# Kernel optimization log

Measured on AMD Instinct MI355X. Metric: run time of the kernel, lower is better.

Reference implementation:

```python
import jax, jax.numpy as jnp
import numpy as np


def _deform_unfold(feat, offset):
    """Deformable 3x3 unfold with bilinear sampling, zero padding outside.
    feat: [B,C,H,W], offset: [B,2K,H,W] (y,x per point). Returns [B,C,K,H,W]."""
    B, C, H, W = feat.shape
    K = offset.shape[1] // 2
    off = offset.reshape(B, K, 2, H, W)
    # 3x3 kernel grid, dilation 1, padding 1 -> relative taps in {-1,0,1}
    ky = (jnp.arange(K) // 3 - 1).astype(feat.dtype)
    kx = (jnp.arange(K) % 3 - 1).astype(feat.dtype)
    hh = jnp.arange(H, dtype=feat.dtype)
    ww = jnp.arange(W, dtype=feat.dtype)
    py = hh[None, None, :, None] + ky[None, :, None, None] + off[:, :, 0]  # [B,K,H,W]
    px = ww[None, None, None, :] + kx[None, :, None, None] + off[:, :, 1]  # [B,K,H,W]
    y0 = jnp.floor(py)
    x0 = jnp.floor(px)
    fy = py - y0  # frac weights
    fx = px - x0
    y0i = y0.astype(jnp.int32)
    x0i = x0.astype(jnp.int32)

    def gather(yi, xi):
        valid = ((yi >= 0) & (yi < H) & (xi >= 0) & (xi < W)).astype(feat.dtype)
        yc = jnp.clip(yi, 0, H - 1)
        xc = jnp.clip(xi, 0, W - 1)
        v = jax.vmap(lambda f, yy, xx: f[:, yy, xx])(feat, yc, xc)  # [B,C,K,H,W]
        return v * valid[:, None]

    w00 = ((1 - fy) * (1 - fx))[:, None]
    w01 = ((1 - fy) * fx)[:, None]
    w10 = (fy * (1 - fx))[:, None]
    w11 = (fy * fx)[:, None]
    return (gather(y0i, x0i) * w00 + gather(y0i, x0i + 1) * w01 +
            gather(y0i + 1, x0i) * w10 + gather(y0i + 1, x0i + 1) * w11)


def setup_inputs() -> dict:
    key = jax.random.key(0)
    ks = jax.random.split(key, 8)
    B, C, H, W = 4, 256, 64, 64
    Ci, P = 128, 9
    x = jax.random.normal(ks[0], (B, C, H, W), jnp.float32)
    offset = jax.random.normal(ks[1], (B, 2 * P, H, W), jnp.float32)
    std = 0.01  # normal_init(std=0.01)
    Wq = jax.random.normal(ks[2], (Ci, C), jnp.float32) * std
    Wk = jax.random.normal(ks[3], (Ci, C), jnp.float32) * std
    Wv = jax.random.normal(ks[4], (Ci, C), jnp.float32) * std
    Wo = jax.random.normal(ks[5], (Ci,), jnp.float32) * std
    bq = jnp.zeros((Ci,), jnp.float32)
    bk = jnp.zeros((Ci,), jnp.float32)
    bv = jnp.zeros((Ci,), jnp.float32)
    bo = jnp.zeros((1,), jnp.float32)
    return {"x": x, "offset": offset, "Wq": Wq, "bq": bq, "Wk": Wk, "bk": bk,
            "Wv": Wv, "bv": bv, "Wo": Wo, "bo": bo}


def reference(x, offset, Wq, bq, Wk, bk, Wv, bv, Wo, bo):
    # 1x1 conv projections
    q = jnp.einsum('bchw,oc->bohw', x, Wq) + bq[None, :, None, None]
    k = jnp.einsum('bchw,oc->bohw', x, Wk) + bk[None, :, None, None]
    v = jnp.einsum('bchw,oc->bohw', x, Wv) + bv[None, :, None, None]
    qu = _deform_unfold(q, offset)  # [B,Ci,K,H,W]
    ku = _deform_unfold(k, offset)  # [B,Ci,K,H,W]
    vu = _deform_unfold(v, offset)  # [B,Ci,K,H,W]
    # per-pixel KxK attention: query [K,Ci] @ key [Ci,K]
    scores = jnp.einsum('bcihw,bcjhw->bijhw', qu, ku)  # [B,K,K,H,W]
    attn = jax.nn.softmax(scores, axis=2)
    # attn [K,K] @ value [K,Ci]
    out_v = jnp.einsum('bijhw,bcjhw->bcihw', attn, vu)  # [B,Ci,K,H,W]
    # conv_out: 1x1 conv Ci->1 over the value, then sigmoid -> [B,K,H,W]
    out = jnp.einsum('bcihw,c->bihw', out_v, Wo) + bo[0]
    return jax.nn.sigmoid(out)
```

## Files before the change

### kernel.cpp

```cpp
#include <hip/hip_runtime.h>

typedef unsigned short u16;
typedef unsigned int u32;

#define B_   4
#define C_   256
#define CI_  128
#define H_   64
#define W_   64
#define NPB_ 4096
#define NP_  16384
#define K_   9
#define MROWS_ 272

typedef __attribute__((ext_vector_type(8))) __bf16 bf16x8_t;
typedef __attribute__((ext_vector_type(4))) float f32x4_t;
typedef __attribute__((ext_vector_type(2))) float f32x2_t;
typedef __attribute__((ext_vector_type(4))) u32 u32x4;

#define GLD(dst, p, immstr) \
    asm volatile("global_load_dwordx4 %0, %1, off offset:" immstr \
                 : "=v"(dst) : "v"(p))

__device__ __forceinline__ float bf2f_lo(u32 w) {
    union { u32 i; float f; } x; x.i = w << 16; return x.f;
}
__device__ __forceinline__ float bf2f_hi(u32 w) {
    union { u32 i; float f; } x; x.i = w & 0xffff0000u; return x.f;
}
__device__ __forceinline__ u16 f2bf(float f) {
    union { float f; u32 i; } x; x.f = f;
    u32 lsb = (x.i >> 16) & 1u;
    return (u16)((x.i + 0x7fffu + lsb) >> 16);
}
__device__ __forceinline__ void acc8p(f32x2_t* f, u32x4 v, f32x2_t w2) {
    f32x2_t p;
    p.x = bf2f_lo(v[0]); p.y = bf2f_hi(v[0]); f[0] += w2 * p;
    p.x = bf2f_lo(v[1]); p.y = bf2f_hi(v[1]); f[1] += w2 * p;
    p.x = bf2f_lo(v[2]); p.y = bf2f_hi(v[2]); f[2] += w2 * p;
    p.x = bf2f_lo(v[3]); p.y = bf2f_hi(v[3]); f[3] += w2 * p;
}

__global__ void k0b_prep(const float* __restrict__ Wq, const float* __restrict__ bq,
                         const float* __restrict__ Wk, const float* __restrict__ bk,
                         const float* __restrict__ Wv, const float* __restrict__ bv,
                         const float* __restrict__ Wo,
                         u16* __restrict__ Wt, float* __restrict__ bias) {
    const int o = blockIdx.x;
    const int c = threadIdx.x;
    u16 val;
    if (o < 128) {
        val = f2bf(Wq[o * C_ + c]);
        if (c == 0) bias[o] = bq[o];
    } else if (o < 256) {
        val = f2bf(Wk[(o - 128) * C_ + c]);
        if (c == 0) bias[o] = bk[o - 128];
    } else if (o == 256) {
        float s = 0.f;
        #pragma unroll 8
        for (int oo = 0; oo < CI_; ++oo)
            s += Wo[oo] * Wv[oo * C_ + c];
        val = f2bf(s);
        if (c == 0) {
            float ts = 0.f;
            #pragma unroll 8
            for (int oo = 0; oo < CI_; ++oo) ts += Wo[oo] * bv[oo];
            bias[256] = ts;
        }
    } else {
        val = 0;
        if (c == 0) bias[o] = 0.f;
    }
    const int mt = o >> 4, l16 = o & 15;
    const int kk = c >> 5, g = (c >> 3) & 3, e = c & 7;
    Wt[(size_t)((mt * 8 + kk) * 64 + g * 16 + l16) * 8 + e] = val;
}

__global__ __launch_bounds__(512) void k1_proj(
    const float* __restrict__ x, const u16* __restrict__ Wt,
    const float* __restrict__ bias,
    u16* __restrict__ qk, float* __restrict__ vs) {
    __shared__ u16 xs[16][272];
    const int t = threadIdx.x;
    const int l = t & 63;
    const int w = t >> 6;
    const int lane16 = l & 15;
    const int g = l >> 4;
    const int p0 = blockIdx.x * 16;
    const int b = p0 >> 12;
    const int pin = p0 & 4095;

    const int mts[3] = {2 * w, 2 * w + 1, 16};

    u32x4 afr[8][3];
    #pragma unroll
    for (int n = 0; n < 3; ++n) {
        const u16* pA = Wt + ((size_t)(mts[n] * 8) * 64 + l) * 8;
        const u16* pB = pA + 4 * 64 * 8;
        GLD(afr[0][n], pA, "0");    GLD(afr[1][n], pA, "1024");
        GLD(afr[2][n], pA, "2048"); GLD(afr[3][n], pA, "3072");
        GLD(afr[4][n], pB, "0");    GLD(afr[5][n], pB, "1024");
        GLD(afr[6][n], pB, "2048"); GLD(afr[7][n], pB, "3072");
    }

    {
        const int spx = t & 15, cg = t >> 4;
        const float* src = x + (size_t)(b * C_ + cg * 8) * NPB_ + pin + spx;
        float v[8];
        #pragma unroll
        for (int i = 0; i < 8; ++i) v[i] = src[(size_t)i * NPB_];
        uint4 pk;
        pk.x = (u32)f2bf(v[0]) | ((u32)f2bf(v[1]) << 16);
        pk.y = (u32)f2bf(v[2]) | ((u32)f2bf(v[3]) << 16);
        pk.z = (u32)f2bf(v[4]) | ((u32)f2bf(v[5]) << 16);
        pk.w = (u32)f2bf(v[6]) | ((u32)f2bf(v[7]) << 16);
        *reinterpret_cast<uint4*>(&xs[spx][cg * 8]) = pk;
    }
    __syncthreads();
    asm volatile("s_waitcnt vmcnt(0)" ::: "memory");
    __builtin_amdgcn_sched_barrier(0);

    f32x4_t acc[3];
    #pragma unroll
    for (int n = 0; n < 3; ++n)
        #pragma unroll
        for (int r = 0; r < 4; ++r)
            acc[n][r] = bias[mts[n] * 16 + g * 4 + r];

    #pragma unroll
    for (int kk = 0; kk < 8; ++kk) {
        const bf16x8_t bv = *reinterpret_cast<const bf16x8_t*>(&xs[lane16][kk * 32 + g * 8]);
        #pragma unroll
        for (int n = 0; n < 3; ++n) {
            const bf16x8_t av = __builtin_bit_cast(bf16x8_t, afr[kk][n]);
            acc[n] = __builtin_amdgcn_mfma_f32_16x16x32_bf16(av, bv, acc[n], 0, 0, 0);
        }
    }

    const int px = p0 + lane16;
    u16* qrow = qk + (size_t)px * C_;
    #pragma unroll
    for (int n = 0; n < 2; ++n) {
        const int mt = mts[n];
        u32* dst = reinterpret_cast<u32*>(qrow + mt * 16 + g * 4);
        dst[0] = (u32)f2bf(acc[n][0]) | ((u32)f2bf(acc[n][1]) << 16);
        dst[1] = (u32)f2bf(acc[n][2]) | ((u32)f2bf(acc[n][3]) << 16);
    }
    if (w == 0 && g == 0) vs[px] = acc[2][0];
}

__global__ __launch_bounds__(256) void k2_attn(
    const float* __restrict__ off, const u16* __restrict__ qk,
    const float* __restrict__ vs, const float* __restrict__ bo,
    float* __restrict__ out) {
    __shared__ f32x4_t red[3][64];
    const int t = threadIdx.x;
    const int l = t & 63;
    const int w = t >> 6;
    const int bid = blockIdx.x;
    const int pixel = (bid & 7) * (NP_ / 8) + (bid >> 3);
    const int b = pixel >> 12;
    const int rem = pixel & 4095;
    const int y = rem >> 6, xx = rem & 63;
    const int l16 = l & 15;
    const int tap = (l16 < K_) ? l16 : (K_ - 1);
    const int g = l >> 4;

    const float* offb = off + ((size_t)b * (2 * K_) + 2 * tap) * NPB_ + rem;
    const float oy = offb[0];
    const float ox = offb[NPB_];
    const float py = (float)(y + tap / 3 - 1) + oy;
    const float px = (float)(xx + tap % 3 - 1) + ox;
    const float fy0 = floorf(py), fx0 = floorf(px);
    const float fy = py - fy0, fx = px - fx0;
    const int y0 = (int)fy0, x0 = (int)fx0;

    const u16* qkbase = qk + ((size_t)(b << 12)) * C_ + w * 32 + g * 8;
    const float* vsm = vs + (b << 12);

    float wgt[4];
    int ppc[4];
    const u16* bp[4];
    #pragma unroll
    for (int c = 0; c < 4; ++c) {
        const int dy = c >> 1, dx = c & 1;
        const int yi = y0 + dy, xi = x0 + dx;
        const float wv = (dy ? fy : 1.f - fy) * (dx ? fx : 1.f - fx);
        const int ok = (yi >= 0) & (yi < H_) & (xi >= 0) & (xi < W_);
        const int yc = min(max(yi, 0), H_ - 1);
        const int xc = min(max(xi, 0), W_ - 1);
        ppc[c] = yc * W_ + xc;
        wgt[c] = ok ? wv : 0.f;
        bp[c] = qkbase + (size_t)ppc[c] * C_;
    }

    u32x4 gq[4], gk[4];
    #pragma unroll
    for (int c = 0; c < 4; ++c) {
        GLD(gq[c], bp[c], "0");
        GLD(gk[c], bp[c], "256");
    }
    float vsc[4];
    if (w == 0) {
        #pragma unroll
        for (int c = 0; c < 4; ++c) vsc[c] = vsm[ppc[c]];
    }
    asm volatile("s_waitcnt vmcnt(0)" ::: "memory");
    __builtin_amdgcn_sched_barrier(0);

    f32x2_t fq[4], fk[4];
    #pragma unroll
    for (int e = 0; e < 4; ++e) { fq[e] = (f32x2_t){0.f, 0.f}; fk[e] = (f32x2_t){0.f, 0.f}; }
    #pragma unroll
    for (int c = 0; c < 4; ++c) {
        const f32x2_t w2 = {wgt[c], wgt[c]};
        acc8p(fq, gq[c], w2);
        acc8p(fk, gk[c], w2);
    }

    bf16x8_t av, bv;
    #pragma unroll
    for (int e = 0; e < 4; ++e) {
        av[2 * e]     = (__bf16)fk[e].x;
        av[2 * e + 1] = (__bf16)fk[e].y;
        bv[2 * e]     = (__bf16)fq[e].x;
        bv[2 * e + 1] = (__bf16)fq[e].y;
    }
    f32x4_t acc = {0.f, 0.f, 0.f, 0.f};
    acc = __builtin_amdgcn_mfma_f32_16x16x32_bf16(av, bv, acc, 0, 0, 0);

    if (w > 0) red[w - 1][l] = acc;
    __syncthreads();
    if (w != 0) return;

    acc += red[0][l];
    acc += red[1][l];
    acc += red[2][l];

    const float vsu_t = wgt[0] * vsc[0] + wgt[1] * vsc[1] +
                        wgt[2] * vsc[2] + wgt[3] * vsc[3];

    float mx = -1e30f;
    #pragma unroll
    for (int r = 0; r < 4; ++r) {
        const int j = g * 4 + r;
        if (j < K_) mx = fmaxf(mx, acc[r]);
    }
    mx = fmaxf(mx, __shfl_xor(mx, 16, 64));
    mx = fmaxf(mx, __shfl_xor(mx, 32, 64));

    float vj[4];
    #pragma unroll
    for (int r = 0; r < 4; ++r) vj[r] = __shfl(vsu_t, g * 4 + r, 64);

    float den = 0.f, num = 0.f;
    #pragma unroll
    for (int r = 0; r < 4; ++r) {
        const int j = g * 4 + r;
        if (j < K_) {
            const float e = __expf(acc[r] - mx);
            den += e;
            num += e * vj[r];
        }
    }
    den += __shfl_xor(den, 16, 64); den += __shfl_xor(den, 32, 64);
    num += __shfl_xor(num, 16, 64); num += __shfl_xor(num, 32, 64);

    if (l < K_) {
        const float z = num / den + bo[0];
        out[(size_t)b * K_ * NPB_ + (size_t)l * NPB_ + rem] = 1.f / (1.f + __expf(-z));
    }
}

extern "C" void kernel_launch(void* const* d_in, const int* in_sizes, int n_in,
                              void* d_out, int out_size, void* d_ws, size_t ws_size,
                              hipStream_t stream) {
    const float* x   = (const float*)d_in[0];
    const float* off = (const float*)d_in[1];
    const float* Wq  = (const float*)d_in[2];
    const float* bq  = (const float*)d_in[3];
    const float* Wk  = (const float*)d_in[4];
    const float* bk  = (const float*)d_in[5];
    const float* Wv  = (const float*)d_in[6];
    const float* bv  = (const float*)d_in[7];
    const float* Wo  = (const float*)d_in[8];
    const float* bo  = (const float*)d_in[9];
    float* out = (float*)d_out;

    char* ws = (char*)d_ws;
    u16*   qkbuf = (u16*)(ws + 4096);
    float* vsmap = (float*)(ws + 4096 + 8388608);
    u16*   Wt    = (u16*)(ws + 4096 + 8388608 + 65536);
    float* bias  = (float*)(ws + 4096 + 8388608 + 65536 + 139264);

    k0b_prep<<<MROWS_, 256, 0, stream>>>(Wq, bq, Wk, bk, Wv, bv, Wo, Wt, bias);
    k1_proj<<<NP_ / 16, 512, 0, stream>>>(x, Wt, bias, qkbuf, vsmap);
    k2_attn<<<NP_, 256, 0, stream>>>(off, qkbuf, vsmap, bo, out);
}
```

Before: 77.11 us.

## Tile attention kernel over 4x8 pixel blocks with LDS-staged channel-chunked q/k window

The q/k buffer is re-laid out into four channel chunks of 64 (32 q and 32 k channels each). The attention kernel now runs one block per 4x8 pixel tile instead of one block per pixel. Each block stages a 16x20 window of each chunk into shared memory and precomputes the bilinear geometry per pixel and tap. Samples outside the window fall back to global loads. This replaces many scattered global gathers with reuse from shared memory, at the cost of far fewer blocks (512), four chunk passes with barriers, and more registers per thread.

```diff
diff --git a/kernel.cpp b/kernel.cpp
--- a/kernel.cpp
+++ b/kernel.cpp
@@ -12,6 +12,13 @@
 #define NP_  16384
 #define K_   9
 #define MROWS_ 272
+
+#define TH_  4
+#define TW_  8
+#define WH_  16
+#define WW_  20
+#define WPX_ (WH_ * WW_)
+#define CROW_ 68
 
 typedef __attribute__((ext_vector_type(8))) __bf16 bf16x8_t;
 typedef __attribute__((ext_vector_type(4))) float f32x4_t;
@@ -79,7 +86,7 @@
 __global__ __launch_bounds__(512) void k1_proj(
     const float* __restrict__ x, const u16* __restrict__ Wt,
     const float* __restrict__ bias,
-    u16* __restrict__ qk, float* __restrict__ vs) {
+    u16* __restrict__ qkc, float* __restrict__ vs) {
     __shared__ u16 xs[16][272];
     const int t = threadIdx.x;
     const int l = t & 63;
@@ -138,137 +145,184 @@
     }
 
     const int px = p0 + lane16;
-    u16* qrow = qk + (size_t)px * C_;
     #pragma unroll
     for (int n = 0; n < 2; ++n) {
         const int mt = mts[n];
-        u32* dst = reinterpret_cast<u32*>(qrow + mt * 16 + g * 4);
-        dst[0] = (u32)f2bf(acc[n][0]) | ((u32)f2bf(acc[n][1]) << 16);
-        dst[1] = (u32)f2bf(acc[n][2]) | ((u32)f2bf(acc[n][3]) << 16);
+        const u32 lo_ = (u32)f2bf(acc[n][0]) | ((u32)f2bf(acc[n][1]) << 16);
+        const u32 hi_ = (u32)f2bf(acc[n][2]) | ((u32)f2bf(acc[n][3]) << 16);
+        int chunk, base;
+        if (mt < 8) { chunk = mt >> 1; base = (mt & 1) * 16 + g * 4; }
+        else { const int m8 = mt - 8; chunk = m8 >> 1; base = 32 + (m8 & 1) * 16 + g * 4; }
+        u32* dst = reinterpret_cast<u32*>(qkc + ((size_t)(chunk * NP_ + px)) * 64 + base);
+        dst[0] = lo_; dst[1] = hi_;
     }
     if (w == 0 && g == 0) vs[px] = acc[2][0];
 }
 
 __global__ __launch_bounds__(256) void k2_attn(
-    const float* __restrict__ off, const u16* __restrict__ qk,
+    const float* __restrict__ off, const u16* __restrict__ qkc,
     const float* __restrict__ vs, const float* __restrict__ bo,
     float* __restrict__ out) {
-    __shared__ f32x4_t red[3][64];
+    __shared__ u16 cb[WPX_ * CROW_];
+    __shared__ u32 geo[32][9][8];
+    __shared__ float vsl[WPX_];
+
     const int t = threadIdx.x;
     const int l = t & 63;
     const int w = t >> 6;
     const int bid = blockIdx.x;
-    const int pixel = (bid & 7) * (NP_ / 8) + (bid >> 3);
-    const int b = pixel >> 12;
-    const int rem = pixel & 4095;
-    const int y = rem >> 6, xx = rem & 63;
+    const int tid = (bid & 7) * 64 + (bid >> 3);
+    const int b = tid >> 7;
+    const int rr = tid & 127;
+    const int ty0 = (rr >> 3) * TH_;
+    const int tx0 = (rr & 7) * TW_;
+    const int y0w = min(max(ty0 - 6, 0), H_ - WH_);
+    const int x0w = min(max(tx0 - 6, 0), W_ - WW_);
+
+    for (int i = t; i < WPX_; i += 256) {
+        const int gy = y0w + i / WW_, gx = x0w + i % WW_;
+        vsl[i] = vs[(b << 12) + gy * W_ + gx];
+    }
+    for (int e = t; e < 32 * K_; e += 256) {
+        const int px = e / K_, tap = e - px * K_;
+        const int y = ty0 + (px >> 3), x = tx0 + (px & 7);
+        const int rem = y * W_ + x;
+        const float* offb = off + ((size_t)b * (2 * K_) + 2 * tap) * NPB_ + rem;
+        const float oy = offb[0], ox = offb[NPB_];
+        const float pyf = (float)(y + tap / 3 - 1) + oy;
+        const float pxf = (float)(x + tap % 3 - 1) + ox;
+        const float fy0 = floorf(pyf), fx0 = floorf(pxf);
+        const float fy = pyf - fy0, fx = pxf - fx0;
+        const int y0 = (int)fy0, x0 = (int)fx0;
+        #pragma unroll
+        for (int c = 0; c < 4; ++c) {
+            const int dy = c >> 1, dx = c & 1;
+            const int yi = y0 + dy, xi = x0 + dx;
+            const float wv = (dy ? fy : 1.f - fy) * (dx ? fx : 1.f - fx);
+            const int ok = (yi >= 0) & (yi < H_) & (xi >= 0) & (xi < W_);
+            const int yc = min(max(yi, 0), H_ - 1);
+            const int xc = min(max(xi, 0), W_ - 1);
+            const int wy = yc - y0w, wx = xc - x0w;
+            const int in = ((unsigned)wy < WH_) & ((unsigned)wx < WW_);
+            const u32 idx = in ? (u32)(wy * WW_ + wx) : 0xFFFFu;
+            union { float f; u32 i; } wb; wb.f = ok ? wv : 0.f;
+            geo[px][tap][2 * c]     = (idx << 16) | (u32)(yc * W_ + xc);
+            geo[px][tap][2 * c + 1] = wb.i;
+        }
+    }
+    __syncthreads();
+
     const int l16 = l & 15;
     const int tap = (l16 < K_) ? l16 : (K_ - 1);
     const int g = l >> 4;
 
-    const float* offb = off + ((size_t)b * (2 * K_) + 2 * tap) * NPB_ + rem;
-    const float oy = offb[0];
-    const float ox = offb[NPB_];
-    const float py = (float)(y + tap / 3 - 1) + oy;
-    const float px = (float)(xx + tap % 3 - 1) + ox;
-    const float fy0 = floorf(py), fx0 = floorf(px);
-    const float fy = py - fy0, fx = px - fx0;
-    const int y0 = (int)fy0, x0 = (int)fx0;
-
-    const u16* qkbase = qk + ((size_t)(b << 12)) * C_ + w * 32 + g * 8;
-    const float* vsm = vs + (b << 12);
-
-    float wgt[4];
-    int ppc[4];
-    const u16* bp[4];
-    #pragma unroll
+    f32x4_t acc[8];
+    float vsu[8];
+    #pragma unroll
+    for (int ps = 0; ps < 8; ++ps) {
+        acc[ps] = (f32x4_t){0.f, 0.f, 0.f, 0.f};
+        vsu[ps] = 0.f;
+    }
+
     for (int c = 0; c < 4; ++c) {
-        const int dy = c >> 1, dx = c & 1;
-        const int yi = y0 + dy, xi = x0 + dx;
-        const float wv = (dy ? fy : 1.f - fy) * (dx ? fx : 1.f - fx);
-        const int ok = (yi >= 0) & (yi < H_) & (xi >= 0) & (xi < W_);
-        const int yc = min(max(yi, 0), H_ - 1);
-        const int xc = min(max(xi, 0), W_ - 1);
-        ppc[c] = yc * W_ + xc;
-        wgt[c] = ok ? wv : 0.f;
-        bp[c] = qkbase + (size_t)ppc[c] * C_;
-    }
-
-    u32x4 gq[4], gk[4];
-    #pragma unroll
-    for (int c = 0; c < 4; ++c) {
-        GLD(gq[c], bp[c], "0");
-        GLD(gk[c], bp[c], "256");
-    }
-    float vsc[4];
-    if (w == 0) {
-        #pragma unroll
-        for (int c = 0; c < 4; ++c) vsc[c] = vsm[ppc[c]];
-    }
-    asm volatile("s_waitcnt vmcnt(0)" ::: "memory");
-    __builtin_amdgcn_sched_barrier(0);
-
-    f32x2_t fq[4], fk[4];
-    #pragma unroll
-    for (int e = 0; e < 4; ++e) { fq[e] = (f32x2_t){0.f, 0.f}; fk[e] = (f32x2_t){0.f, 0.f}; }
-    #pragma unroll
-    for (int c = 0; c < 4; ++c) {
-        const f32x2_t w2 = {wgt[c], wgt[c]};
-        acc8p(fq, gq[c], w2);
-        acc8p(fk, gk[c], w2);
-    }
-
-    bf16x8_t av, bv;
-    #pragma unroll
-    for (int e = 0; e < 4; ++e) {
-        av[2 * e]     = (__bf16)fk[e].x;
-        av[2 * e + 1] = (__bf16)fk[e].y;
-        bv[2 * e]     = (__bf16)fq[e].x;
-        bv[2 * e + 1] = (__bf16)fq[e].y;
-    }
-    f32x4_t acc = {0.f, 0.f, 0.f, 0.f};
-    acc = __builtin_amdgcn_mfma_f32_16x16x32_bf16(av, bv, acc, 0, 0, 0);
-
-    if (w > 0) red[w - 1][l] = acc;
-    __syncthreads();
-    if (w != 0) return;
-
-    acc += red[0][l];
-    acc += red[1][l];
-    acc += red[2][l];
-
-    const float vsu_t = wgt[0] * vsc[0] + wgt[1] * vsc[1] +
-                        wgt[2] * vsc[2] + wgt[3] * vsc[3];
-
-    float mx = -1e30f;
-    #pragma unroll
-    for (int r = 0; r < 4; ++r) {
-        const int j = g * 4 + r;
-        if (j < K_) mx = fmaxf(mx, acc[r]);
-    }
-    mx = fmaxf(mx, __shfl_xor(mx, 16, 64));
-    mx = fmaxf(mx, __shfl_xor(mx, 32, 64));
-
-    float vj[4];
-    #pragma unroll
-    for (int r = 0; r < 4; ++r) vj[r] = __shfl(vsu_t, g * 4 + r, 64);
-
-    float den = 0.f, num = 0.f;
-    #pragma unroll
-    for (int r = 0; r < 4; ++r) {
-        const int j = g * 4 + r;
-        if (j < K_) {
-            const float e = __expf(acc[r] - mx);
-            den += e;
-            num += e * vj[r];
-        }
-    }
-    den += __shfl_xor(den, 16, 64); den += __shfl_xor(den, 32, 64);
-    num += __shfl_xor(num, 16, 64); num += __shfl_xor(num, 32, 64);
-
-    if (l < K_) {
-        const float z = num / den + bo[0];
-        out[(size_t)b * K_ * NPB_ + (size_t)l * NPB_ + rem] = 1.f / (1.f + __expf(-z));
+        for (int i = t; i < WPX_ * 2; i += 256) {
+            const int wp = i >> 1, half = i & 1;
+            const int gy = y0w + wp / WW_, gx = x0w + wp % WW_;
+            const u16* src = qkc + ((size_t)(c * NP_ + (b << 12) + gy * W_ + gx)) * 64 + half * 32;
+            const uint4 v0 = *reinterpret_cast<const uint4*>(src);
+            const uint4 v1 = *reinterpret_cast<const uint4*>(src + 8);
+            const uint4 v2 = *reinterpret_cast<const uint4*>(src + 16);
+            const uint4 v3 = *reinterpret_cast<const uint4*>(src + 24);
+            u16* d = &cb[wp * CROW_ + half * 32];
+            *reinterpret_cast<uint4*>(d) = v0;
+            *reinterpret_cast<uint4*>(d + 8) = v1;
+            *reinterpret_cast<uint4*>(d + 16) = v2;
+            *reinterpret_cast<uint4*>(d + 24) = v3;
+        }
+        __syncthreads();
+
+        #pragma unroll
+        for (int ps = 0; ps < 8; ++ps) {
+            const int local = w * 8 + ps;
+            const u32x4 ge0 = *reinterpret_cast<const u32x4*>(&geo[local][tap][0]);
+            const u32x4 ge1 = *reinterpret_cast<const u32x4*>(&geo[local][tap][4]);
+            f32x2_t fq[4], fk[4];
+            #pragma unroll
+            for (int e = 0; e < 4; ++e) { fq[e] = (f32x2_t){0.f, 0.f}; fk[e] = (f32x2_t){0.f, 0.f}; }
+            #pragma unroll
+            for (int cn = 0; cn < 4; ++cn) {
+                const u32 gi_w = (cn < 2) ? ge0[2 * cn] : ge1[2 * (cn - 2)];
+                union { u32 i; float f; } wb;
+                wb.i = (cn < 2) ? ge0[2 * cn + 1] : ge1[2 * (cn - 2) + 1];
+                const float wv = wb.f;
+                const u32 idx = gi_w >> 16;
+                u32x4 qv, kv;
+                if (idx != 0xFFFFu) {
+                    const u16* p = &cb[idx * CROW_ + g * 8];
+                    qv = *reinterpret_cast<const u32x4*>(p);
+                    kv = *reinterpret_cast<const u32x4*>(p + 32);
+                    if (c == 0) vsu[ps] += wv * vsl[idx];
+                } else {
+                    const u32 gp = gi_w & 0xFFFFu;
+                    const u16* p = qkc + ((size_t)(c * NP_ + (b << 12) + gp)) * 64 + g * 8;
+                    qv = *reinterpret_cast<const u32x4*>(p);
+                    kv = *reinterpret_cast<const u32x4*>(p + 32);
+                    if (c == 0) vsu[ps] += wv * vs[(b << 12) + gp];
+                }
+                const f32x2_t w2 = {wv, wv};
+                acc8p(fq, qv, w2);
+                acc8p(fk, kv, w2);
+            }
+            bf16x8_t av, bv;
+            #pragma unroll
+            for (int e = 0; e < 4; ++e) {
+                av[2 * e]     = (__bf16)fk[e].x;
+                av[2 * e + 1] = (__bf16)fk[e].y;
+                bv[2 * e]     = (__bf16)fq[e].x;
+                bv[2 * e + 1] = (__bf16)fq[e].y;
+            }
+            acc[ps] = __builtin_amdgcn_mfma_f32_16x16x32_bf16(av, bv, acc[ps], 0, 0, 0);
+        }
+        __syncthreads();
+    }
+
+    const float bof = bo[0];
+    #pragma unroll
+    for (int ps = 0; ps < 8; ++ps) {
+        const int local = w * 8 + ps;
+        const int y = ty0 + (local >> 3), x = tx0 + (local & 7);
+        const int rem = y * W_ + x;
+
+        float mx = -1e30f;
+        #pragma unroll
+        for (int r = 0; r < 4; ++r) {
+            const int j = g * 4 + r;
+            if (j < K_) mx = fmaxf(mx, acc[ps][r]);
+        }
+        mx = fmaxf(mx, __shfl_xor(mx, 16, 64));
+        mx = fmaxf(mx, __shfl_xor(mx, 32, 64));
+
+        float vj[4];
+        #pragma unroll
+        for (int r = 0; r < 4; ++r) vj[r] = __shfl(vsu[ps], g * 4 + r, 64);
+
+        float den = 0.f, num = 0.f;
+        #pragma unroll
+        for (int r = 0; r < 4; ++r) {
+            const int j = g * 4 + r;
+            if (j < K_) {
+                const float e = __expf(acc[ps][r] - mx);
+                den += e;
+                num += e * vj[r];
+            }
+        }
+        den += __shfl_xor(den, 16, 64); den += __shfl_xor(den, 32, 64);
+        num += __shfl_xor(num, 16, 64); num += __shfl_xor(num, 32, 64);
+
+        if (l < K_) {
+            const float z = num / den + bof;
+            out[(size_t)b * K_ * NPB_ + (size_t)l * NPB_ + rem] = 1.f / (1.f + __expf(-z));
+        }
     }
 }
 
@@ -288,12 +342,12 @@
     float* out = (float*)d_out;
 
     char* ws = (char*)d_ws;
-    u16*   qkbuf = (u16*)(ws + 4096);
+    u16*   qkc   = (u16*)(ws + 4096);
     float* vsmap = (float*)(ws + 4096 + 8388608);
     u16*   Wt    = (u16*)(ws + 4096 + 8388608 + 65536);
     float* bias  = (float*)(ws + 4096 + 8388608 + 65536 + 139264);
 
     k0b_prep<<<MROWS_, 256, 0, stream>>>(Wq, bq, Wk, bk, Wv, bv, Wo, Wt, bias);
-    k1_proj<<<NP_ / 16, 512, 0, stream>>>(x, Wt, bias, qkbuf, vsmap);
-    k2_attn<<<NP_, 256, 0, stream>>>(off, qkbuf, vsmap, bo, out);
-}
+    k1_proj<<<NP_ / 16, 512, 0, stream>>>(x, Wt, bias, qkc, vsmap);
+    k2_attn<<<512, 256, 0, stream>>>(off, qkc, vsmap, bo, out);
+}
```

After: 101.7 us. 1.32x slower.
